# Performance work log

Measured on AMD Instinct MI355X. Metric: run time of the kernel, lower is better.

## Reference

```python
import jax, jax.numpy as jnp
import numpy as np

S, B, H = 2048, 32, 1024

def setup_inputs() -> dict:
    key = jax.random.key(0)
    k1, k2, k3, k4 = jax.random.split(key, 4)
    scale = 1.0 / np.sqrt(H)
    hidden = jax.random.normal(k1, (B, H), dtype=jnp.float32)
    encoder_outputs = jax.random.normal(k2, (S, B, H), dtype=jnp.float32)
    W = jax.random.normal(k3, (H, H), dtype=jnp.float32) * scale  # nn.Linear weight [out,in]
    b = jax.random.normal(k4, (H,), dtype=jnp.float32) * scale    # nn.Linear bias
    return {"hidden": hidden, "encoder_outputs": encoder_outputs, "W": W, "b": b}

def reference(hidden, encoder_outputs, W, b):
    # method == 'general': energy[s,b] = W @ encoder_outputs[s,b] + b
    # score[b,s] = hidden[b] . energy[s,b]
    energy = jnp.einsum('sbh,oh->sbo', encoder_outputs, W) + b  # [S,B,H]
    attn_energies = jnp.einsum('bh,sbh->bs', hidden, energy)    # [B,S]
    # F.softmax on a 2D tensor defaults to dim=1 (over seq)
    attn = jax.nn.softmax(attn_energies, axis=1)
    return attn[:, None, :]  # [B,1,S]
```

## Files before the change

kernel.cpp:

```cpp
#include <hip/hip_runtime.h>
#include <math.h>

#define SS 2048
#define BB 32
#define HH 1024
#define OCH 16
#define OLEN (HH/OCH)

typedef float v4f __attribute__((ext_vector_type(4)));

__global__ __launch_bounds__(256) void vmat_kernel(const float* __restrict__ hidden,
                                                   const float* __restrict__ W,
                                                   float* __restrict__ vpart) {
    const int oc = blockIdx.x;
    const int b  = blockIdx.y;
    const int t  = threadIdx.x;
    const float* __restrict__ hrow = hidden + (size_t)b * HH;
    const v4f* __restrict__ Wrow = (const v4f*)W;

    v4f acc = (v4f){0.f, 0.f, 0.f, 0.f};
    const int o0 = oc * OLEN;
    #pragma unroll 4
    for (int oo = 0; oo < OLEN; ++oo) {
        const int o = o0 + oo;
        const float hs = hrow[o];
        const v4f w = Wrow[(size_t)o * 256 + t];
        acc += hs * w;
    }
    ((v4f*)(vpart + ((size_t)oc * BB + b) * HH))[t] = acc;
}

__global__ __launch_bounds__(256) void fold_kernel(const float* __restrict__ vpart,
                                                   float* __restrict__ v) {
    const int b = blockIdx.x;
    const int t = threadIdx.x;
    v4f acc = (v4f){0.f, 0.f, 0.f, 0.f};
    #pragma unroll
    for (int c = 0; c < OCH; ++c)
        acc += ((const v4f*)(vpart + ((size_t)c * BB + b) * HH))[t];
    ((v4f*)(v + (size_t)b * HH))[t] = acc;
}

__global__ __launch_bounds__(256, 4) void score_kernel(const float* __restrict__ enc,
                                                       const float* __restrict__ v,
                                                       float* __restrict__ out) {
    const int b = blockIdx.x;
    const int wave = threadIdx.x >> 6;
    const int lane = threadIdx.x & 63;

    const v4f* __restrict__ vrow = (const v4f*)(v + (size_t)b * HH);
    const v4f v0 = vrow[lane];
    const v4f v1 = vrow[lane + 64];
    const v4f v2 = vrow[lane + 128];
    const v4f v3 = vrow[lane + 192];

    const int s0 = (blockIdx.y * 4 + wave) * 4;
    const v4f* __restrict__ erow0 =
        (const v4f*)(enc + ((size_t)s0 * BB + b) * HH);
    const size_t sstride = (size_t)BB * HH / 4;

    v4f e[4][4];
    #pragma unroll
    for (int r = 0; r < 4; ++r) {
        const v4f* __restrict__ p = erow0 + (size_t)r * sstride;
        e[r][0] = __builtin_nontemporal_load(&p[lane]);
        e[r][1] = __builtin_nontemporal_load(&p[lane + 64]);
        e[r][2] = __builtin_nontemporal_load(&p[lane + 128]);
        e[r][3] = __builtin_nontemporal_load(&p[lane + 192]);
    }

    #pragma unroll
    for (int r = 0; r < 4; ++r) {
        float acc = 0.f;
        acc = fmaf(e[r][0].x, v0.x, acc); acc = fmaf(e[r][0].y, v0.y, acc);
        acc = fmaf(e[r][0].z, v0.z, acc); acc = fmaf(e[r][0].w, v0.w, acc);
        acc = fmaf(e[r][1].x, v1.x, acc); acc = fmaf(e[r][1].y, v1.y, acc);
        acc = fmaf(e[r][1].z, v1.z, acc); acc = fmaf(e[r][1].w, v1.w, acc);
        acc = fmaf(e[r][2].x, v2.x, acc); acc = fmaf(e[r][2].y, v2.y, acc);
        acc = fmaf(e[r][2].z, v2.z, acc); acc = fmaf(e[r][2].w, v2.w, acc);
        acc = fmaf(e[r][3].x, v3.x, acc); acc = fmaf(e[r][3].y, v3.y, acc);
        acc = fmaf(e[r][3].z, v3.z, acc); acc = fmaf(e[r][3].w, v3.w, acc);

        #pragma unroll
        for (int off = 32; off >= 1; off >>= 1)
            acc += __shfl_xor(acc, off, 64);

        if (lane == 0) out[(size_t)b * SS + s0 + r] = acc;
    }
}

__global__ __launch_bounds__(256) void softmax_kernel(float* __restrict__ out) {
    const int b = blockIdx.x;
    float* __restrict__ row = out + (size_t)b * SS;
    const int tid = threadIdx.x;
    const int wave = tid >> 6;
    const int lane = tid & 63;

    float x[8];
    float m = -INFINITY;
    #pragma unroll
    for (int i = 0; i < 8; ++i) {
        x[i] = row[tid + 256 * i];
        m = fmaxf(m, x[i]);
    }
    #pragma unroll
    for (int off = 32; off >= 1; off >>= 1)
        m = fmaxf(m, __shfl_xor(m, off, 64));

    __shared__ float redm[4];
    __shared__ float reds[4];
    if (lane == 0) redm[wave] = m;
    __syncthreads();
    m = fmaxf(fmaxf(redm[0], redm[1]), fmaxf(redm[2], redm[3]));

    float ssum = 0.f;
    #pragma unroll
    for (int i = 0; i < 8; ++i) {
        x[i] = expf(x[i] - m);
        ssum += x[i];
    }
    #pragma unroll
    for (int off = 32; off >= 1; off >>= 1)
        ssum += __shfl_xor(ssum, off, 64);
    if (lane == 0) reds[wave] = ssum;
    __syncthreads();
    ssum = (reds[0] + reds[1]) + (reds[2] + reds[3]);

    const float inv = 1.0f / ssum;
    #pragma unroll
    for (int i = 0; i < 8; ++i)
        row[tid + 256 * i] = x[i] * inv;
}

extern "C" void kernel_launch(void* const* d_in, const int* in_sizes, int n_in,
                              void* d_out, int out_size, void* d_ws, size_t ws_size,
                              hipStream_t stream) {
    const float* hidden = (const float*)d_in[0];
    const float* enc    = (const float*)d_in[1];
    const float* W      = (const float*)d_in[2];
    float* out   = (float*)d_out;
    float* vpart = (float*)d_ws;
    float* v     = vpart + (size_t)OCH * BB * HH;

    vmat_kernel<<<dim3(OCH, BB), 256, 0, stream>>>(hidden, W, vpart);
    fold_kernel<<<BB, 256, 0, stream>>>(vpart, v);
    score_kernel<<<dim3(BB, SS / 16), 256, 0, stream>>>(enc, v, out);
    softmax_kernel<<<BB, 256, 0, stream>>>(out);
}
```

Measured before the change: 353.2 us.

## Fuse partial-sum fold and softmax into score kernel via last-block counter

Removes the separate fold and softmax launches. Each score block now sums the 16 partial v vectors itself into LDS before its dot products. The last block per batch row, found with an atomic counter reset by vmat_kernel, performs the row softmax. This saves two kernel launches and a global round trip for v, but every one of the 4096 blocks redundantly re-reads 64 KB of partials and adds fences and atomics.

```diff
diff --git a/kernel.cpp b/kernel.cpp
--- a/kernel.cpp
+++ b/kernel.cpp
@@ -6,15 +6,20 @@
 #define HH 1024
 #define OCH 16
 #define OLEN (HH/OCH)
+#define NYB (SS/16)
+#define CNT_STRIDE 16
 
 typedef float v4f __attribute__((ext_vector_type(4)));
 
 __global__ __launch_bounds__(256) void vmat_kernel(const float* __restrict__ hidden,
                                                    const float* __restrict__ W,
-                                                   float* __restrict__ vpart) {
+                                                   float* __restrict__ vpart,
+                                                   int* __restrict__ cnt) {
     const int oc = blockIdx.x;
     const int b  = blockIdx.y;
     const int t  = threadIdx.x;
+    if (oc == 0 && b == 0 && t < BB) cnt[t * CNT_STRIDE] = 0;
+
     const float* __restrict__ hrow = hidden + (size_t)b * HH;
     const v4f* __restrict__ Wrow = (const v4f*)W;
 
@@ -30,29 +35,33 @@
     ((v4f*)(vpart + ((size_t)oc * BB + b) * HH))[t] = acc;
 }
 
-__global__ __launch_bounds__(256) void fold_kernel(const float* __restrict__ vpart,
-                                                   float* __restrict__ v) {
+__global__ __launch_bounds__(256, 4) void score_fused_kernel(const float* __restrict__ enc,
+                                                             const float* __restrict__ vpart,
+                                                             float* __restrict__ out,
+                                                             int* __restrict__ cnt) {
     const int b = blockIdx.x;
     const int t = threadIdx.x;
-    v4f acc = (v4f){0.f, 0.f, 0.f, 0.f};
-    #pragma unroll
-    for (int c = 0; c < OCH; ++c)
-        acc += ((const v4f*)(vpart + ((size_t)c * BB + b) * HH))[t];
-    ((v4f*)(v + (size_t)b * HH))[t] = acc;
-}
+    const int wave = t >> 6;
+    const int lane = t & 63;
 
-__global__ __launch_bounds__(256, 4) void score_kernel(const float* __restrict__ enc,
-                                                       const float* __restrict__ v,
-                                                       float* __restrict__ out) {
-    const int b = blockIdx.x;
-    const int wave = threadIdx.x >> 6;
-    const int lane = threadIdx.x & 63;
+    __shared__ float vlds[HH];
+    __shared__ float redm[4];
+    __shared__ float reds[4];
+    __shared__ int last;
 
-    const v4f* __restrict__ vrow = (const v4f*)(v + (size_t)b * HH);
-    const v4f v0 = vrow[lane];
-    const v4f v1 = vrow[lane + 64];
-    const v4f v2 = vrow[lane + 128];
-    const v4f v3 = vrow[lane + 192];
+    {
+        v4f facc = (v4f){0.f, 0.f, 0.f, 0.f};
+        #pragma unroll
+        for (int c = 0; c < OCH; ++c)
+            facc += ((const v4f*)(vpart + ((size_t)c * BB + b) * HH))[t];
+        ((v4f*)vlds)[t] = facc;
+    }
+    __syncthreads();
+
+    const v4f v0 = ((const v4f*)vlds)[lane];
+    const v4f v1 = ((const v4f*)vlds)[lane + 64];
+    const v4f v2 = ((const v4f*)vlds)[lane + 128];
+    const v4f v3 = ((const v4f*)vlds)[lane + 192];
 
     const int s0 = (blockIdx.y * 4 + wave) * 4;
     const v4f* __restrict__ erow0 =
@@ -87,28 +96,24 @@
 
         if (lane == 0) out[(size_t)b * SS + s0 + r] = acc;
     }
-}
 
-__global__ __launch_bounds__(256) void softmax_kernel(float* __restrict__ out) {
-    const int b = blockIdx.x;
+    __threadfence();
+    if (t == 0) last = atomicAdd(&cnt[b * CNT_STRIDE], 1);
+    __syncthreads();
+    if (last != NYB - 1) return;
+    __threadfence();
+
     float* __restrict__ row = out + (size_t)b * SS;
-    const int tid = threadIdx.x;
-    const int wave = tid >> 6;
-    const int lane = tid & 63;
-
     float x[8];
     float m = -INFINITY;
     #pragma unroll
     for (int i = 0; i < 8; ++i) {
-        x[i] = row[tid + 256 * i];
+        x[i] = row[t + 256 * i];
         m = fmaxf(m, x[i]);
     }
     #pragma unroll
     for (int off = 32; off >= 1; off >>= 1)
         m = fmaxf(m, __shfl_xor(m, off, 64));
-
-    __shared__ float redm[4];
-    __shared__ float reds[4];
     if (lane == 0) redm[wave] = m;
     __syncthreads();
     m = fmaxf(fmaxf(redm[0], redm[1]), fmaxf(redm[2], redm[3]));
@@ -129,7 +134,7 @@
     const float inv = 1.0f / ssum;
     #pragma unroll
     for (int i = 0; i < 8; ++i)
-        row[tid + 256 * i] = x[i] * inv;
+        row[t + 256 * i] = x[i] * inv;
 }
 
 extern "C" void kernel_launch(void* const* d_in, const int* in_sizes, int n_in,
@@ -140,10 +145,8 @@
     const float* W      = (const float*)d_in[2];
     float* out   = (float*)d_out;
     float* vpart = (float*)d_ws;
-    float* v     = vpart + (size_t)OCH * BB * HH;
+    int*   cnt   = (int*)(vpart + (size_t)OCH * BB * HH);
 
-    vmat_kernel<<<dim3(OCH, BB), 256, 0, stream>>>(hidden, W, vpart);
-    fold_kernel<<<BB, 256, 0, stream>>>(vpart, v);
-    score_kernel<<<dim3(BB, SS / 16), 256, 0, stream>>>(enc, v, out);
-    softmax_kernel<<<BB, 256, 0, stream>>>(out);
+    vmat_kernel<<<dim3(OCH, BB), 256, 0, stream>>>(hidden, W, vpart, cnt);
+    score_fused_kernel<<<dim3(BB, NYB), 256, 0, stream>>>(enc, vpart, out, cnt);
 }
```

Result: slower. 1.103 ms (+212.3%).
